# Kernel optimization log

Measured on AMD Instinct MI355X. Metric: run time of the kernel, lower is better.

Reference implementation:

```python
import jax, jax.numpy as jnp
import numpy as np

B, M, C, D, FF, FEAT = 1, 1024, 128, 512, 1024, 20
PAIR = 3 * D + 2 * FEAT  # slow_scorer_size = 1576


def _ffnn(x, W0, b0, W1, b1):
    # FFNN(depth=1): hidden relu layer then linear output (eval mode, no dropout)
    return jax.nn.relu(x @ W0 + b0) @ W1 + b1


def _batch_gather(x, idx):
    # x: [B, M, ...], idx: [B, ...] int -> gather along mention dim per batch
    return jax.vmap(lambda xb, ib: xb[ib])(x, idx)


def _bucket_distance(d):
    # log-scale distance buckets 0..9 (identity for d<=4)
    log_idx = jnp.floor(jnp.log(jnp.maximum(d, 1).astype(jnp.float32)) / jnp.log(2.0)).astype(jnp.int32) + 3
    return jnp.clip(jnp.where(d <= 4, d, log_idx), 0, 9)


def setup_inputs() -> dict:
    key = jax.random.key(0)
    ks = jax.random.split(key, 10)
    s = 0.02
    return {
        'mention_emb': jax.random.normal(ks[0], (B, M, D), dtype=jnp.float32),
        'mention_cluster_ids': jax.random.randint(ks[1], (B, M), 0, 200),
        'mention_speaker_ids': jax.random.randint(ks[2], (B, M), 0, 2),
        'ms_W0': jax.random.normal(ks[3], (D, FF), dtype=jnp.float32) * s,
        'ms_b0': jnp.zeros((FF,), jnp.float32),
        'ms_W1': jax.random.normal(ks[4], (FF, 1), dtype=jnp.float32) * s,
        'ms_b1': jnp.zeros((1,), jnp.float32),
        'sp_W0': jax.random.normal(ks[5], (PAIR, FF), dtype=jnp.float32) * s,
        'sp_b0': jnp.zeros((FF,), jnp.float32),
        'sp_W1': jax.random.normal(ks[6], (FF, 1), dtype=jnp.float32) * s,
        'sp_b1': jnp.zeros((1,), jnp.float32),
        'speaker_emb': jax.random.normal(ks[7], (2, FEAT), dtype=jnp.float32) * s,
        'bucket_emb': jax.random.normal(ks[8], (10, FEAT), dtype=jnp.float32) * s,
    }


def reference(mention_emb, mention_cluster_ids, mention_speaker_ids,
              ms_W0, ms_b0, ms_W1, ms_b1,
              sp_W0, sp_b0, sp_W1, sp_b1,
              speaker_emb, bucket_emb):
    # mention scoring
    mention_scores = _ffnn(mention_emb, ms_W0, ms_b0, ms_W1, ms_b1)[..., 0]  # [B, M]

    # get_antecedent_info: fixed window of C previous mentions
    offsets = jnp.arange(1, C + 1)[None, None, :]                    # [1,1,C]
    raw = jnp.arange(M)[None, :, None] - offsets                      # [1,M,C]
    antecedents = jnp.broadcast_to(jnp.clip(raw, 0, M - 1), (B, M, C))
    ant_mask = jnp.broadcast_to(raw >= 0, (B, M, C))

    fast_scores = _batch_gather(mention_scores, antecedents) + mention_scores[:, :, None]
    antecedent_emb = _batch_gather(mention_emb, antecedents)          # [B,M,C,D]

    # slow pair scorer features
    same_speaker = (_batch_gather(mention_speaker_ids, antecedents) == mention_speaker_ids[:, :, None]).astype(jnp.int32)
    speaker_feat = speaker_emb[same_speaker]                          # [B,M,C,FEAT]
    bucket_feat = jnp.broadcast_to(bucket_emb[_bucket_distance(offsets)], (B, M, C, FEAT))

    src = jnp.broadcast_to(mention_emb[:, :, None, :], (B, M, C, D))
    pair_emb = jnp.concatenate([src, antecedent_emb, src * antecedent_emb, speaker_feat, bucket_feat], axis=-1)
    slow_scores = _ffnn(pair_emb, sp_W0, sp_b0, sp_W1, sp_b1)[..., 0]  # [B,M,C]

    antecedent_scores = fast_scores + slow_scores + jnp.log(ant_mask.astype(jnp.float32))
    overall_scores = jnp.concatenate([jnp.zeros((B, M, 1), jnp.float32), antecedent_scores], axis=2)
    overall_dist = jax.nn.softmax(overall_scores, axis=-1)
    eps = 1e-6
    overall_dist = jnp.clip(overall_dist, eps, 1.0 - eps)
    overall_dist = overall_dist / jnp.sum(overall_dist, axis=-1, keepdims=True)

    # coref loss from cluster ids
    ant_cluster = _batch_gather(mention_cluster_ids, antecedents) * ant_mask.astype(mention_cluster_ids.dtype)
    same_cluster = ant_cluster == mention_cluster_ids[:, :, None]
    non_dummy = (mention_cluster_ids > 0)[:, :, None]
    ant_labels = same_cluster & non_dummy
    dummy_labels = ~jnp.any(ant_labels, axis=2, keepdims=True)
    overall_labels = jnp.concatenate([dummy_labels, ant_labels], axis=2)
    loss = -jnp.sum(jnp.log(overall_dist) * overall_labels.astype(jnp.float32), axis=2)
    loss = jnp.mean(jnp.sum(loss, axis=1))
    return overall_dist, loss
```

## Files before the change

kernel.cpp:

```cpp
#include <hip/hip_runtime.h>
#include <math.h>

#define MM 1024
#define DD 512
#define CC 128
#define LDSR 516


typedef __attribute__((ext_vector_type(8))) short bf16x8;
typedef __attribute__((ext_vector_type(4), aligned(8))) short bf16x4a;
typedef __attribute__((ext_vector_type(4))) float f32x4;
typedef __attribute__((ext_vector_type(16))) float f32x16;

__device__ __forceinline__ ushort bf16_rn(float x) {
    uint u = __float_as_uint(x);
    uint r = u + 0x7fffu + ((u >> 16) & 1u);
    return (ushort)(r >> 16);
}
__device__ __forceinline__ float bf16_to_f(ushort u) {
    return __uint_as_float(((uint)u) << 16);
}
__device__ __forceinline__ bf16x8 ld_lds16(const ushort* p) {
    bf16x4a lo = *(const bf16x4a*)p;
    bf16x4a hi = *(const bf16x4a*)(p + 4);
    return __builtin_shufflevector(lo, hi, 0, 1, 2, 3, 4, 5, 6, 7);
}

__global__ __launch_bounds__(256) void prep_emb(const float* __restrict__ emb,
                                                ushort* __restrict__ embb)
{
    int i = blockIdx.x * 256 + threadIdx.x;
    float2 v = ((const float2*)emb)[i];
    ushort2 o;
    o.x = bf16_rn(v.x);
    o.y = bf16_rn(v.y);
    ((ushort2*)embb)[i] = o;
}

__global__ __launch_bounds__(256) void prep_wall(const float* __restrict__ ms_W0,
                                                 const float* __restrict__ sp_W0,
                                                 ushort* __restrict__ Wall)
{
    __shared__ float t[64][65];
    const int k0 = blockIdx.x * 64;
    const int n0 = blockIdx.y * 64;
    const int g = n0 >> 10;
    const float* src = (g == 0) ? ms_W0 : (sp_W0 + (size_t)(g - 1) * 512 * 1024);
    const int col0 = n0 & 1023;
    const int tr = threadIdx.x >> 6, tc = threadIdx.x & 63;
#pragma unroll
    for (int i = 0; i < 16; ++i) {
        int k = tr + i * 4;
        t[k][tc] = src[(size_t)(k0 + k) * 1024 + col0 + tc];
    }
    __syncthreads();
    const int f = threadIdx.x >> 2;
    const int c4 = threadIdx.x & 3;
    ushort tmp[16];
#pragma unroll
    for (int j = 0; j < 16; ++j) tmp[j] = bf16_rn(t[c4 * 16 + j][f]);
    uint4* dst = (uint4*)(Wall + (size_t)(n0 + f) * 512 + k0 + c4 * 16);
    dst[0] = *(uint4*)&tmp[0];
    dst[1] = *(uint4*)&tmp[8];
}

__global__ __launch_bounds__(64) void prep_wfrag(const float* __restrict__ W,
                                                 ushort* __restrict__ dst_frag)
{
    const int ts = blockIdx.x;
    const int l = threadIdx.x;
    const int tt = ts >> 5, s = ts & 31;
    const int f = tt * 32 + (l & 31);
    const int kb = s * 16 + (l >> 5) * 8;
    ushort tmp[8];
#pragma unroll
    for (int j = 0; j < 8; ++j) tmp[j] = bf16_rn(W[(size_t)(kb + j) * 1024 + f]);
    uint4* dst = (uint4*)(dst_frag + ((size_t)ts * 64 + l) * 8);
    *dst = *(uint4*)&tmp[0];
}

__global__ __launch_bounds__(256) void gemm_h_mfma(
    const ushort* __restrict__ embb, const ushort* __restrict__ Wall,
    float* __restrict__ H)
{
    const int n0 = blockIdx.x * 128;
    const int m0 = blockIdx.y * 128;
    const int lane = threadIdx.x & 63, wave = threadIdx.x >> 6;
    const int wx = wave & 1, wy = wave >> 1;
    const int l15 = lane & 15, lq = lane >> 4;

    const ushort* arow[4];
#pragma unroll
    for (int mi = 0; mi < 4; ++mi)
        arow[mi] = embb + (size_t)(m0 + wy * 64 + mi * 16 + l15) * 512;
    const ushort* brow[4];
#pragma unroll
    for (int ni = 0; ni < 4; ++ni)
        brow[ni] = Wall + (size_t)(n0 + wx * 64 + ni * 16 + l15) * 512;

    f32x4 acc[4][4];
#pragma unroll
    for (int i = 0; i < 4; ++i)
#pragma unroll
        for (int j = 0; j < 4; ++j) acc[i][j] = (f32x4)0.f;

    for (int kt = 0; kt < 512; kt += 32) {
        const int ko = kt + lq * 8;
        bf16x8 av[4], bv[4];
#pragma unroll
        for (int mi = 0; mi < 4; ++mi) av[mi] = *(const bf16x8*)(arow[mi] + ko);
#pragma unroll
        for (int ni = 0; ni < 4; ++ni) bv[ni] = *(const bf16x8*)(brow[ni] + ko);
#pragma unroll
        for (int mi = 0; mi < 4; ++mi)
#pragma unroll
            for (int ni = 0; ni < 4; ++ni)
                acc[mi][ni] = __builtin_amdgcn_mfma_f32_16x16x32_bf16(av[mi], bv[ni], acc[mi][ni], 0, 0, 0);
    }
#pragma unroll
    for (int mi = 0; mi < 4; ++mi)
#pragma unroll
        for (int r = 0; r < 4; ++r) {
            int mrow = m0 + wy * 64 + mi * 16 + lq * 4 + r;
#pragma unroll
            for (int ni = 0; ni < 4; ++ni)
                H[(size_t)mrow * 3072 + n0 + wx * 64 + ni * 16 + l15] = acc[mi][ni][r];
        }
}

__global__ void small_proj(const float* __restrict__ speaker_emb,
                           const float* __restrict__ bucket_emb,
                           const float* __restrict__ sp_W0,
                           float* __restrict__ spk_proj, float* __restrict__ bkt_proj)
{
    int r = blockIdx.x;
    const float* e; const float* W; float* out;
    if (r < 2) { e = speaker_emb + r * 20; W = sp_W0 + (size_t)1536 * 1024; out = spk_proj + r * 1024; }
    else       { e = bucket_emb + (r - 2) * 20; W = sp_W0 + (size_t)1556 * 1024; out = bkt_proj + (r - 2) * 1024; }
    float ek[20];
#pragma unroll
    for (int k = 0; k < 20; ++k) ek[k] = e[k];
    for (int f = threadIdx.x; f < 1024; f += blockDim.x) {
        float s = 0.f;
#pragma unroll
        for (int k = 0; k < 20; ++k) s = fmaf(ek[k], W[(size_t)k * 1024 + f], s);
        out[f] = s;
    }
}

__global__ __launch_bounds__(256) void mention_score(
    const float* __restrict__ H, const float* __restrict__ ms_b0,
    const float* __restrict__ ms_W1, const float* __restrict__ ms_b1,
    float* __restrict__ ms)
{
    int m = blockIdx.x;
    float v = 0.f;
    for (int f = threadIdx.x; f < 1024; f += 256) {
        float h = H[(size_t)m * 3072 + f] + ms_b0[f];
        v += fmaxf(h, 0.f) * ms_W1[f];
    }
#pragma unroll
    for (int o = 1; o < 64; o <<= 1) v += __shfl_xor(v, o);
    __shared__ float sm[4];
    if ((threadIdx.x & 63) == 0) sm[threadIdx.x >> 6] = v;
    __syncthreads();
    if (threadIdx.x == 0) ms[m] = sm[0] + sm[1] + sm[2] + sm[3] + ms_b1[0];
}

__global__ __launch_bounds__(512, 4) void pair_mfma(
    const ushort* __restrict__ embb, const ushort* __restrict__ Wfrag,
    const float* __restrict__ H, const float* __restrict__ spk_proj,
    const float* __restrict__ bkt_proj, const float* __restrict__ sp_b0,
    const float* __restrict__ sp_W1, const int* __restrict__ speaker,
    float* __restrict__ slow0, float* __restrict__ slow1)
{
    extern __shared__ ushort Alds[];
    float* red = (float*)(Alds + 64 * LDSR);
    int* meta_ss = (int*)(red + 8 * 64);
    int* meta_bk = meta_ss + 64;
    const int m = blockIdx.x;
    const int cbase = (blockIdx.y & 1) * 64;
    const int fh = blockIdx.y >> 1;
    const int tid = threadIdx.x;
    const int spk_m = speaker[m];

    {
        const int c = tid & 63;
        const int kh = (tid >> 6) * 64;
        int a = m - 1 - (cbase + c); if (a < 0) a = 0;
        const ushort* ea = embb + (size_t)a * 512 + kh;
        const ushort* em = embb + (size_t)m * 512 + kh;
        ushort* dst = Alds + c * LDSR + kh;
#pragma unroll
        for (int j = 0; j < 64; j += 8) {
            bf16x8 va = *(const bf16x8*)(ea + j);
            bf16x8 vm = *(const bf16x8*)(em + j);
            uint pr[4];
#pragma unroll
            for (int p = 0; p < 4; ++p) {
                float q0 = bf16_to_f((ushort)va[2 * p])     * bf16_to_f((ushort)vm[2 * p]);
                float q1 = bf16_to_f((ushort)va[2 * p + 1]) * bf16_to_f((ushort)vm[2 * p + 1]);
                pr[p] = __builtin_amdgcn_perm(__float_as_uint(q1), __float_as_uint(q0), 0x07060302u);
            }
            *(uint2*)(dst + j)     = *(uint2*)&pr[0];
            *(uint2*)(dst + j + 4) = *(uint2*)&pr[2];
        }
        if (tid < 64) {
            meta_ss[c] = (speaker[a] == spk_m) ? 1 : 0;
            int off = cbase + c + 1;
            int bk;
            if (off <= 4) bk = off;
            else { bk = 31 - __clz(off) + 3; if (bk > 9) bk = 9; }
            meta_bk[c] = bk;
        }
    }
    __syncthreads();

    const int lane = tid & 63;
    const int wave = __builtin_amdgcn_readfirstlane(tid >> 6);
    const int l31 = lane & 31, k5 = lane >> 5;

    const int f0 = fh * 512 + wave * 64;
    const ushort* bb = Wfrag + (size_t)(fh * 16 + wave * 2) * 16384 + (size_t)lane * 8;
    const ushort* ab = Alds + l31 * LDSR + k5 * 8;

    f32x16 acc[2][2];
#pragma unroll
    for (int i = 0; i < 2; ++i)
#pragma unroll
        for (int j = 0; j < 2; ++j) acc[i][j] = (f32x16)0.f;

#pragma unroll 2
    for (int s = 0; s < 32; ++s) {
        bf16x8 b0 = *(const bf16x8*)(bb + s * 512);
        bf16x8 b1 = *(const bf16x8*)(bb + 16384 + s * 512);
        bf16x8 a0 = ld_lds16(ab + s * 16);
        bf16x8 a1 = ld_lds16(ab + 32 * LDSR + s * 16);
        __builtin_amdgcn_s_setprio(1);
        acc[0][0] = __builtin_amdgcn_mfma_f32_32x32x16_bf16(a0, b0, acc[0][0], 0, 0, 0);
        acc[0][1] = __builtin_amdgcn_mfma_f32_32x32x16_bf16(a0, b1, acc[0][1], 0, 0, 0);
        acc[1][0] = __builtin_amdgcn_mfma_f32_32x32x16_bf16(a1, b0, acc[1][0], 0, 0, 0);
        acc[1][1] = __builtin_amdgcn_mfma_f32_32x32x16_bf16(a1, b1, acc[1][1], 0, 0, 0);
        __builtin_amdgcn_s_setprio(0);
    }

    float srcb[2], w1v[2], sp0v[2], sp1v[2];
#pragma unroll
    for (int ni = 0; ni < 2; ++ni) {
        int fcol = f0 + ni * 32 + l31;
        srcb[ni] = H[(size_t)m * 3072 + 1024 + fcol] + sp_b0[fcol];
        w1v[ni]  = sp_W1[fcol];
        sp0v[ni] = spk_proj[fcol];
        sp1v[ni] = spk_proj[1024 + fcol];
    }
#pragma unroll
    for (int mi = 0; mi < 2; ++mi) {
#pragma unroll
        for (int reg = 0; reg < 16; ++reg) {
            const int c = mi * 32 + 4 * k5 + (reg & 3) + 8 * (reg >> 2);
            int a = m - 1 - (cbase + c); if (a < 0) a = 0;
            const int ss = meta_ss[c];
            const int bk = meta_bk[c];
            const float* antp = H + (size_t)a * 3072 + 2048;
            float s = 0.f;
#pragma unroll
            for (int ni = 0; ni < 2; ++ni) {
                const int fcol = f0 + ni * 32 + l31;
                float bval = bkt_proj[(size_t)bk * 1024 + fcol];
                float pre = acc[mi][ni][reg] + srcb[ni] + antp[fcol] + (ss ? sp1v[ni] : sp0v[ni]) + bval;
                s += fmaxf(pre, 0.f) * w1v[ni];
            }
            s += __shfl_xor(s, 1); s += __shfl_xor(s, 2); s += __shfl_xor(s, 4);
            s += __shfl_xor(s, 8); s += __shfl_xor(s, 16);
            if (l31 == 0) red[wave * 64 + c] = s;
        }
    }
    __syncthreads();
    if (tid < 64) {
        float s = 0.f;
#pragma unroll
        for (int i = 0; i < 8; ++i) s += red[i * 64 + tid];
        float* sout = fh ? slow1 : slow0;
        sout[(size_t)m * 128 + cbase + tid] = s;
    }
}

__device__ __forceinline__ float bsum2(float v, float* sm) {
#pragma unroll
    for (int o = 1; o < 64; o <<= 1) v += __shfl_xor(v, o);
    __syncthreads();
    if ((threadIdx.x & 63) == 0) sm[threadIdx.x >> 6] = v;
    __syncthreads();
    return sm[0] + sm[1];
}
__device__ __forceinline__ float bmax2(float v, float* sm) {
#pragma unroll
    for (int o = 1; o < 64; o <<= 1) v = fmaxf(v, __shfl_xor(v, o));
    __syncthreads();
    if ((threadIdx.x & 63) == 0) sm[threadIdx.x >> 6] = v;
    __syncthreads();
    return fmaxf(sm[0], sm[1]);
}

__global__ __launch_bounds__(128) void softmax_loss(
    const float* __restrict__ slow0, const float* __restrict__ slow1,
    const float* __restrict__ ms,
    const float* __restrict__ sp_b1, const int* __restrict__ cluster,
    float* __restrict__ out, float* __restrict__ loss_partial)
{
    const int m = blockIdx.x, c = threadIdx.x;
    __shared__ float sm[2];
    const int raw = m - 1 - c;
    const bool maskv = raw >= 0;
    const int a = maskv ? raw : 0;
    float score = slow0[(size_t)m * 128 + c] + slow1[(size_t)m * 128 + c]
                + sp_b1[0] + ms[m] + ms[a];
    if (!maskv) score = -INFINITY;

    float mx = fmaxf(bmax2(score, sm), 0.f);
    float e = expf(score - mx);
    float e0 = expf(0.f - mx);
    float sum = bsum2(e, sm) + e0;
    float p = e / sum, p0 = e0 / sum;
    const float eps = 1e-6f;
    p  = fminf(fmaxf(p,  eps), 1.f - eps);
    p0 = fminf(fmaxf(p0, eps), 1.f - eps);
    float sum2 = bsum2(p, sm) + p0;
    p /= sum2; p0 /= sum2;
    out[(size_t)m * 129 + 1 + c] = p;
    if (c == 0) out[(size_t)m * 129] = p0;

    const int cid = cluster[m];
    const bool lbl = maskv && (cid > 0) && (cluster[a] == cid);
    float anyc = bsum2(lbl ? 1.f : 0.f, sm);
    float lsum = bsum2(lbl ? -logf(p) : 0.f, sm);
    if (c == 0) {
        if (anyc == 0.f) lsum += -logf(p0);
        loss_partial[m] = lsum;
    }
}

__global__ void loss_sum(const float* __restrict__ lp, float* __restrict__ out) {
    float v = 0.f;
    for (int i = threadIdx.x; i < 1024; i += 256) v += lp[i];
#pragma unroll
    for (int o = 1; o < 64; o <<= 1) v += __shfl_xor(v, o);
    __shared__ float sm[4];
    if ((threadIdx.x & 63) == 0) sm[threadIdx.x >> 6] = v;
    __syncthreads();
    if (threadIdx.x == 0) out[(size_t)1024 * 129] = sm[0] + sm[1] + sm[2] + sm[3];
}

extern "C" void kernel_launch(void* const* d_in, const int* in_sizes, int n_in,
                              void* d_out, int out_size, void* d_ws, size_t ws_size,
                              hipStream_t stream)
{
    const float* emb   = (const float*)d_in[0];
    const int*   clus  = (const int*)  d_in[1];
    const int*   spk   = (const int*)  d_in[2];
    const float* ms_W0 = (const float*)d_in[3];
    const float* ms_b0 = (const float*)d_in[4];
    const float* ms_W1 = (const float*)d_in[5];
    const float* ms_b1 = (const float*)d_in[6];
    const float* sp_W0 = (const float*)d_in[7];
    const float* sp_b0 = (const float*)d_in[8];
    const float* sp_W1 = (const float*)d_in[9];
    const float* sp_b1 = (const float*)d_in[10];
    const float* spke  = (const float*)d_in[11];
    const float* bkte  = (const float*)d_in[12];

    float* ws = (float*)d_ws;
    float* H        = ws;
    float* slow0    = ws + 3145728;
    float* spk_proj = ws + 3276800;
    float* bkt_proj = ws + 3278848;
    float* msc      = ws + 3289088;
    float* lossp    = ws + 3290112;
    ushort* embb    = (ushort*)(ws + 3291136);
    ushort* Wall    = (ushort*)(ws + 3553280);
    ushort* Wfrag   = Wall + (size_t)3072 * 512;
    float* slow1    = ws + 4601856;
    float* out = (float*)d_out;

    const int pair_lds = 64 * LDSR * 2 + 8 * 64 * 4 + 2 * 64 * 4;

    static bool attr_set = false;
    if (!attr_set) {
        hipFuncSetAttribute((const void*)&pair_mfma,
                            hipFuncAttributeMaxDynamicSharedMemorySize,
                            pair_lds);
        attr_set = true;
    }

    hipLaunchKernelGGL(prep_emb, dim3(1024), dim3(256), 0, stream, emb, embb);
    hipLaunchKernelGGL(prep_wall, dim3(8, 48), dim3(256), 0, stream, ms_W0, sp_W0, Wall);
    hipLaunchKernelGGL(prep_wfrag, dim3(1024), dim3(64), 0, stream,
                       sp_W0 + (size_t)1024 * 1024, Wfrag);
    hipLaunchKernelGGL(gemm_h_mfma, dim3(24, 8), dim3(256), 0, stream, embb, Wall, H);
    hipLaunchKernelGGL(small_proj, dim3(12), dim3(256), 0, stream, spke, bkte, sp_W0, spk_proj, bkt_proj);
    hipLaunchKernelGGL(mention_score, dim3(1024), dim3(256), 0, stream, H, ms_b0, ms_W1, ms_b1, msc);
    hipLaunchKernelGGL(pair_mfma, dim3(1024, 4), dim3(512), pair_lds, stream,
                       embb, Wfrag, H, spk_proj, bkt_proj, sp_b0, sp_W1, spk, slow0, slow1);
    hipLaunchKernelGGL(softmax_loss, dim3(1024), dim3(128), 0, stream,
                       slow0, slow1, msc, sp_b1, clus, out, lossp);
    hipLaunchKernelGGL(loss_sum, dim3(1), dim3(256), 0, stream, lossp, out);
}
```

Before: 367.3 us.

## Merge two antecedent halves into one 1024-thread pair block; widen LDS rows for 16B loads

The pair kernel now has each block handle all 128 antecedents for one mention and feature half, using 16 waves instead of 8, so each wave's W fragment is shared by two wave groups within the block. This halves the grid and the per-block launch/setup overhead. The LDS row pitch changes from 516 to 520 so A-operand reads and writes can be single 16-byte accesses instead of split 8-byte ones. Doubling the block size and LDS footprint (about 140KB) reduces how many blocks fit per CU and may change bank-conflict behavior.

After: 403.0 us. +9.7%, slower.

```diff
diff --git a/kernel.cpp b/kernel.cpp
--- a/kernel.cpp
+++ b/kernel.cpp
@@ -4,11 +4,10 @@
 #define MM 1024
 #define DD 512
 #define CC 128
-#define LDSR 516
+#define LDSR 520
 
 
 typedef __attribute__((ext_vector_type(8))) short bf16x8;
-typedef __attribute__((ext_vector_type(4), aligned(8))) short bf16x4a;
 typedef __attribute__((ext_vector_type(4))) float f32x4;
 typedef __attribute__((ext_vector_type(16))) float f32x16;
 
@@ -21,9 +20,7 @@
     return __uint_as_float(((uint)u) << 16);
 }
 __device__ __forceinline__ bf16x8 ld_lds16(const ushort* p) {
-    bf16x4a lo = *(const bf16x4a*)p;
-    bf16x4a hi = *(const bf16x4a*)(p + 4);
-    return __builtin_shufflevector(lo, hi, 0, 1, 2, 3, 4, 5, 6, 7);
+    return *(const bf16x8*)__builtin_assume_aligned(p, 16);
 }
 
 __global__ __launch_bounds__(256) void prep_emb(const float* __restrict__ emb,
@@ -167,7 +164,7 @@
     if (threadIdx.x == 0) ms[m] = sm[0] + sm[1] + sm[2] + sm[3] + ms_b1[0];
 }
 
-__global__ __launch_bounds__(512, 4) void pair_mfma(
+__global__ __launch_bounds__(1024, 4) void pair_mfma(
     const ushort* __restrict__ embb, const ushort* __restrict__ Wfrag,
     const float* __restrict__ H, const float* __restrict__ spk_proj,
     const float* __restrict__ bkt_proj, const float* __restrict__ sp_b0,
@@ -175,19 +172,18 @@
     float* __restrict__ slow0, float* __restrict__ slow1)
 {
     extern __shared__ ushort Alds[];
-    float* red = (float*)(Alds + 64 * LDSR);
-    int* meta_ss = (int*)(red + 8 * 64);
-    int* meta_bk = meta_ss + 64;
+    float* red = (float*)(Alds + 128 * LDSR);
+    int* meta_ss = (int*)(red + 16 * 64);
+    int* meta_bk = meta_ss + 128;
     const int m = blockIdx.x;
-    const int cbase = (blockIdx.y & 1) * 64;
-    const int fh = blockIdx.y >> 1;
+    const int fh = blockIdx.y;
     const int tid = threadIdx.x;
     const int spk_m = speaker[m];
 
     {
-        const int c = tid & 63;
-        const int kh = (tid >> 6) * 64;
-        int a = m - 1 - (cbase + c); if (a < 0) a = 0;
+        const int c = tid >> 3;
+        const int kh = (tid & 7) * 64;
+        int a = m - 1 - c; if (a < 0) a = 0;
         const ushort* ea = embb + (size_t)a * 512 + kh;
         const ushort* em = embb + (size_t)m * 512 + kh;
         ushort* dst = Alds + c * LDSR + kh;
@@ -202,12 +198,11 @@
                 float q1 = bf16_to_f((ushort)va[2 * p + 1]) * bf16_to_f((ushort)vm[2 * p + 1]);
                 pr[p] = __builtin_amdgcn_perm(__float_as_uint(q1), __float_as_uint(q0), 0x07060302u);
             }
-            *(uint2*)(dst + j)     = *(uint2*)&pr[0];
-            *(uint2*)(dst + j + 4) = *(uint2*)&pr[2];
+            *(uint4*)__builtin_assume_aligned(dst + j, 16) = *(uint4*)&pr[0];
         }
-        if (tid < 64) {
+        if ((tid & 7) == 0) {
             meta_ss[c] = (speaker[a] == spk_m) ? 1 : 0;
-            int off = cbase + c + 1;
+            int off = c + 1;
             int bk;
             if (off <= 4) bk = off;
             else { bk = 31 - __clz(off) + 3; if (bk > 9) bk = 9; }
@@ -218,11 +213,12 @@
 
     const int lane = tid & 63;
     const int wave = __builtin_amdgcn_readfirstlane(tid >> 6);
+    const int wc = wave >> 3, wf = wave & 7;
     const int l31 = lane & 31, k5 = lane >> 5;
 
-    const int f0 = fh * 512 + wave * 64;
-    const ushort* bb = Wfrag + (size_t)(fh * 16 + wave * 2) * 16384 + (size_t)lane * 8;
-    const ushort* ab = Alds + l31 * LDSR + k5 * 8;
+    const int f0 = fh * 512 + wf * 64;
+    const ushort* bb = Wfrag + (size_t)(fh * 16 + wf * 2) * 16384 + (size_t)lane * 8;
+    const ushort* ab = Alds + (wc * 64 + l31) * LDSR + k5 * 8;
 
     f32x16 acc[2][2];
 #pragma unroll
@@ -257,8 +253,9 @@
     for (int mi = 0; mi < 2; ++mi) {
 #pragma unroll
         for (int reg = 0; reg < 16; ++reg) {
-            const int c = mi * 32 + 4 * k5 + (reg & 3) + 8 * (reg >> 2);
-            int a = m - 1 - (cbase + c); if (a < 0) a = 0;
+            const int cl = mi * 32 + 4 * k5 + (reg & 3) + 8 * (reg >> 2);
+            const int c = wc * 64 + cl;
+            int a = m - 1 - c; if (a < 0) a = 0;
             const int ss = meta_ss[c];
             const int bk = meta_bk[c];
             const float* antp = H + (size_t)a * 3072 + 2048;
@@ -272,16 +269,18 @@
             }
             s += __shfl_xor(s, 1); s += __shfl_xor(s, 2); s += __shfl_xor(s, 4);
             s += __shfl_xor(s, 8); s += __shfl_xor(s, 16);
-            if (l31 == 0) red[wave * 64 + c] = s;
+            if (l31 == 0) red[wave * 64 + cl] = s;
         }
     }
     __syncthreads();
-    if (tid < 64) {
+    if (tid < 128) {
+        const int c = tid;
+        const int wcc = c >> 6, cl = c & 63;
         float s = 0.f;
 #pragma unroll
-        for (int i = 0; i < 8; ++i) s += red[i * 64 + tid];
+        for (int i = 0; i < 8; ++i) s += red[(wcc * 8 + i) * 64 + cl];
         float* sout = fh ? slow1 : slow0;
-        sout[(size_t)m * 128 + cbase + tid] = s;
+        sout[(size_t)m * 128 + c] = s;
     }
 }
 
@@ -382,7 +381,7 @@
     float* slow1    = ws + 4601856;
     float* out = (float*)d_out;
 
-    const int pair_lds = 64 * LDSR * 2 + 8 * 64 * 4 + 2 * 64 * 4;
+    const int pair_lds = 128 * LDSR * 2 + 16 * 64 * 4 + 2 * 128 * 4;
 
     static bool attr_set = false;
     if (!attr_set) {
@@ -399,7 +398,7 @@
     hipLaunchKernelGGL(gemm_h_mfma, dim3(24, 8), dim3(256), 0, stream, embb, Wall, H);
     hipLaunchKernelGGL(small_proj, dim3(12), dim3(256), 0, stream, spke, bkte, sp_W0, spk_proj, bkt_proj);
     hipLaunchKernelGGL(mention_score, dim3(1024), dim3(256), 0, stream, H, ms_b0, ms_W1, ms_b1, msc);
-    hipLaunchKernelGGL(pair_mfma, dim3(1024, 4), dim3(512), pair_lds, stream,
+    hipLaunchKernelGGL(pair_mfma, dim3(1024, 2), dim3(1024), pair_lds, stream,
                        embb, Wfrag, H, spk_proj, bkt_proj, sp_b0, sp_W1, spk, slow0, slow1);
     hipLaunchKernelGGL(softmax_loss, dim3(1024), dim3(128), 0, stream,
                        slow0, slow1, msc, sp_b1, clus, out, lossp);
```

## Retile pair kernel to 32-antecedent blocks using 16x16x32 MFMA

Applied to the files above, without the earlier changes.

The pair-scoring kernel now handles 32 antecedents per block instead of 64, doubling the grid, and switches from 32x32x16 to 16x16x32 bf16 MFMA. Weight fragments are repacked to match, and each wave loops over two 32-feature sub-tiles, accumulating into the shared reduction buffer. The goal is smaller LDS and register footprint for higher occupancy (launch bounds raised to 8 blocks) and a cheaper epilogue. The cost is that each weight fragment is now reloaded by twice as many blocks, which adds global/L2 traffic.

Result: no change. 360.8 us (-1.8%).

```diff
diff --git a/kernel.cpp b/kernel.cpp
--- a/kernel.cpp
+++ b/kernel.cpp
@@ -10,7 +10,6 @@
 typedef __attribute__((ext_vector_type(8))) short bf16x8;
 typedef __attribute__((ext_vector_type(4), aligned(8))) short bf16x4a;
 typedef __attribute__((ext_vector_type(4))) float f32x4;
-typedef __attribute__((ext_vector_type(16))) float f32x16;
 
 __device__ __forceinline__ ushort bf16_rn(float x) {
     uint u = __float_as_uint(x);
@@ -64,14 +63,14 @@
     dst[1] = *(uint4*)&tmp[8];
 }
 
-__global__ __launch_bounds__(64) void prep_wfrag(const float* __restrict__ W,
-                                                 ushort* __restrict__ dst_frag)
+__global__ __launch_bounds__(64) void prep_wfrag16(const float* __restrict__ W,
+                                                   ushort* __restrict__ dst_frag)
 {
     const int ts = blockIdx.x;
     const int l = threadIdx.x;
-    const int tt = ts >> 5, s = ts & 31;
-    const int f = tt * 32 + (l & 31);
-    const int kb = s * 16 + (l >> 5) * 8;
+    const int t16 = ts >> 4, s = ts & 15;
+    const int f = t16 * 16 + (l & 15);
+    const int kb = s * 32 + ((l >> 4) & 3) * 8;
     ushort tmp[8];
 #pragma unroll
     for (int j = 0; j < 8; ++j) tmp[j] = bf16_rn(W[(size_t)(kb + j) * 1024 + f]);
@@ -167,32 +166,33 @@
     if (threadIdx.x == 0) ms[m] = sm[0] + sm[1] + sm[2] + sm[3] + ms_b1[0];
 }
 
-__global__ __launch_bounds__(512, 4) void pair_mfma(
-    const ushort* __restrict__ embb, const ushort* __restrict__ Wfrag,
+__global__ __launch_bounds__(512, 8) void pair_mfma(
+    const ushort* __restrict__ embb, const ushort* __restrict__ Wfrag16,
     const float* __restrict__ H, const float* __restrict__ spk_proj,
     const float* __restrict__ bkt_proj, const float* __restrict__ sp_b0,
     const float* __restrict__ sp_W1, const int* __restrict__ speaker,
     float* __restrict__ slow0, float* __restrict__ slow1)
 {
     extern __shared__ ushort Alds[];
-    float* red = (float*)(Alds + 64 * LDSR);
-    int* meta_ss = (int*)(red + 8 * 64);
-    int* meta_bk = meta_ss + 64;
+    float* red = (float*)(Alds + 32 * LDSR);
+    int* meta_ss = (int*)(red + 8 * 32);
+    int* meta_bk = meta_ss + 32;
     const int m = blockIdx.x;
-    const int cbase = (blockIdx.y & 1) * 64;
-    const int fh = blockIdx.y >> 1;
+    const int cq = blockIdx.y & 3;
+    const int fh = blockIdx.y >> 2;
+    const int cbase = cq * 32;
     const int tid = threadIdx.x;
     const int spk_m = speaker[m];
 
     {
-        const int c = tid & 63;
-        const int kh = (tid >> 6) * 64;
+        const int c = tid & 31;
+        const int kh = (tid >> 5) * 32;
         int a = m - 1 - (cbase + c); if (a < 0) a = 0;
         const ushort* ea = embb + (size_t)a * 512 + kh;
         const ushort* em = embb + (size_t)m * 512 + kh;
         ushort* dst = Alds + c * LDSR + kh;
 #pragma unroll
-        for (int j = 0; j < 64; j += 8) {
+        for (int j = 0; j < 32; j += 8) {
             bf16x8 va = *(const bf16x8*)(ea + j);
             bf16x8 vm = *(const bf16x8*)(em + j);
             uint pr[4];
@@ -205,7 +205,7 @@
             *(uint2*)(dst + j)     = *(uint2*)&pr[0];
             *(uint2*)(dst + j + 4) = *(uint2*)&pr[2];
         }
-        if (tid < 64) {
+        if (tid < 32) {
             meta_ss[c] = (speaker[a] == spk_m) ? 1 : 0;
             int off = cbase + c + 1;
             int bk;
@@ -218,68 +218,75 @@
 
     const int lane = tid & 63;
     const int wave = __builtin_amdgcn_readfirstlane(tid >> 6);
-    const int l31 = lane & 31, k5 = lane >> 5;
-
-    const int f0 = fh * 512 + wave * 64;
-    const ushort* bb = Wfrag + (size_t)(fh * 16 + wave * 2) * 16384 + (size_t)lane * 8;
-    const ushort* ab = Alds + l31 * LDSR + k5 * 8;
-
-    f32x16 acc[2][2];
-#pragma unroll
-    for (int i = 0; i < 2; ++i)
-#pragma unroll
-        for (int j = 0; j < 2; ++j) acc[i][j] = (f32x16)0.f;
+    const int l15 = lane & 15, lq = lane >> 4;
+    const ushort* ab0 = Alds + l15 * LDSR + lq * 8;
+
+#pragma unroll 1
+    for (int ft2 = 0; ft2 < 2; ++ft2) {
+        const int f0a = fh * 512 + wave * 64 + ft2 * 32;
+        const ushort* bb0 = Wfrag16 + (size_t)(fh * 32 + wave * 4 + ft2 * 2) * 8192
+                                    + (size_t)lane * 8;
+        f32x4 acc[2][2];
+#pragma unroll
+        for (int i = 0; i < 2; ++i)
+#pragma unroll
+            for (int j = 0; j < 2; ++j) acc[i][j] = (f32x4)0.f;
 
 #pragma unroll 2
-    for (int s = 0; s < 32; ++s) {
-        bf16x8 b0 = *(const bf16x8*)(bb + s * 512);
-        bf16x8 b1 = *(const bf16x8*)(bb + 16384 + s * 512);
-        bf16x8 a0 = ld_lds16(ab + s * 16);
-        bf16x8 a1 = ld_lds16(ab + 32 * LDSR + s * 16);
-        __builtin_amdgcn_s_setprio(1);
-        acc[0][0] = __builtin_amdgcn_mfma_f32_32x32x16_bf16(a0, b0, acc[0][0], 0, 0, 0);
-        acc[0][1] = __builtin_amdgcn_mfma_f32_32x32x16_bf16(a0, b1, acc[0][1], 0, 0, 0);
-        acc[1][0] = __builtin_amdgcn_mfma_f32_32x32x16_bf16(a1, b0, acc[1][0], 0, 0, 0);
-        acc[1][1] = __builtin_amdgcn_mfma_f32_32x32x16_bf16(a1, b1, acc[1][1], 0, 0, 0);
-        __builtin_amdgcn_s_setprio(0);
-    }
-
-    float srcb[2], w1v[2], sp0v[2], sp1v[2];
-#pragma unroll
-    for (int ni = 0; ni < 2; ++ni) {
-        int fcol = f0 + ni * 32 + l31;
-        srcb[ni] = H[(size_t)m * 3072 + 1024 + fcol] + sp_b0[fcol];
-        w1v[ni]  = sp_W1[fcol];
-        sp0v[ni] = spk_proj[fcol];
-        sp1v[ni] = spk_proj[1024 + fcol];
-    }
-#pragma unroll
-    for (int mi = 0; mi < 2; ++mi) {
-#pragma unroll
-        for (int reg = 0; reg < 16; ++reg) {
-            const int c = mi * 32 + 4 * k5 + (reg & 3) + 8 * (reg >> 2);
-            int a = m - 1 - (cbase + c); if (a < 0) a = 0;
-            const int ss = meta_ss[c];
-            const int bk = meta_bk[c];
-            const float* antp = H + (size_t)a * 3072 + 2048;
-            float s = 0.f;
-#pragma unroll
-            for (int ni = 0; ni < 2; ++ni) {
-                const int fcol = f0 + ni * 32 + l31;
-                float bval = bkt_proj[(size_t)bk * 1024 + fcol];
-                float pre = acc[mi][ni][reg] + srcb[ni] + antp[fcol] + (ss ? sp1v[ni] : sp0v[ni]) + bval;
-                s += fmaxf(pre, 0.f) * w1v[ni];
+        for (int s = 0; s < 16; ++s) {
+            bf16x8 b0 = *(const bf16x8*)(bb0 + s * 512);
+            bf16x8 b1 = *(const bf16x8*)(bb0 + 8192 + s * 512);
+            bf16x8 a0 = ld_lds16(ab0 + s * 32);
+            bf16x8 a1 = ld_lds16(ab0 + 16 * LDSR + s * 32);
+            __builtin_amdgcn_s_setprio(1);
+            acc[0][0] = __builtin_amdgcn_mfma_f32_16x16x32_bf16(a0, b0, acc[0][0], 0, 0, 0);
+            acc[0][1] = __builtin_amdgcn_mfma_f32_16x16x32_bf16(a0, b1, acc[0][1], 0, 0, 0);
+            acc[1][0] = __builtin_amdgcn_mfma_f32_16x16x32_bf16(a1, b0, acc[1][0], 0, 0, 0);
+            acc[1][1] = __builtin_amdgcn_mfma_f32_16x16x32_bf16(a1, b1, acc[1][1], 0, 0, 0);
+            __builtin_amdgcn_s_setprio(0);
+        }
+
+        float srcb[2], w1v[2], sp0v[2], sp1v[2];
+#pragma unroll
+        for (int fi = 0; fi < 2; ++fi) {
+            int fcol = f0a + fi * 16 + l15;
+            srcb[fi] = H[(size_t)m * 3072 + 1024 + fcol] + sp_b0[fcol];
+            w1v[fi]  = sp_W1[fcol];
+            sp0v[fi] = spk_proj[fcol];
+            sp1v[fi] = spk_proj[1024 + fcol];
+        }
+#pragma unroll
+        for (int ct = 0; ct < 2; ++ct) {
+#pragma unroll
+            for (int reg = 0; reg < 4; ++reg) {
+                const int cl = ct * 16 + lq * 4 + reg;
+                int a = m - 1 - (cbase + cl); if (a < 0) a = 0;
+                const int ss = meta_ss[cl];
+                const int bk = meta_bk[cl];
+                const float* antp = H + (size_t)a * 3072 + 2048;
+                float s = 0.f;
+#pragma unroll
+                for (int fi = 0; fi < 2; ++fi) {
+                    const int fcol = f0a + fi * 16 + l15;
+                    float bval = bkt_proj[(size_t)bk * 1024 + fcol];
+                    float pre = acc[ct][fi][reg] + srcb[fi] + antp[fcol]
+                              + (ss ? sp1v[fi] : sp0v[fi]) + bval;
+                    s += fmaxf(pre, 0.f) * w1v[fi];
+                }
+                s += __shfl_xor(s, 1); s += __shfl_xor(s, 2);
+                s += __shfl_xor(s, 4); s += __shfl_xor(s, 8);
+                if (l15 == 0) {
+                    if (ft2 == 0) red[wave * 32 + cl] = s;
+                    else          red[wave * 32 + cl] += s;
+                }
             }
-            s += __shfl_xor(s, 1); s += __shfl_xor(s, 2); s += __shfl_xor(s, 4);
-            s += __shfl_xor(s, 8); s += __shfl_xor(s, 16);
-            if (l31 == 0) red[wave * 64 + c] = s;
-        }
-    }
-    __syncthreads();
-    if (tid < 64) {
+        }
+    }
+    __syncthreads();
+    if (tid < 32) {
         float s = 0.f;
 #pragma unroll
-        for (int i = 0; i < 8; ++i) s += red[i * 64 + tid];
+        for (int i = 0; i < 8; ++i) s += red[i * 32 + tid];
         float* sout = fh ? slow1 : slow0;
         sout[(size_t)m * 128 + cbase + tid] = s;
     }
@@ -378,11 +385,11 @@
     float* lossp    = ws + 3290112;
     ushort* embb    = (ushort*)(ws + 3291136);
     ushort* Wall    = (ushort*)(ws + 3553280);
-    ushort* Wfrag   = Wall + (size_t)3072 * 512;
+    ushort* Wfrag16 = Wall + (size_t)3072 * 512;
     float* slow1    = ws + 4601856;
     float* out = (float*)d_out;
 
-    const int pair_lds = 64 * LDSR * 2 + 8 * 64 * 4 + 2 * 64 * 4;
+    const int pair_lds = 32 * LDSR * 2 + 8 * 32 * 4 + 2 * 32 * 4;
 
     static bool attr_set = false;
     if (!attr_set) {
@@ -394,13 +401,13 @@
 
     hipLaunchKernelGGL(prep_emb, dim3(1024), dim3(256), 0, stream, emb, embb);
     hipLaunchKernelGGL(prep_wall, dim3(8, 48), dim3(256), 0, stream, ms_W0, sp_W0, Wall);
-    hipLaunchKernelGGL(prep_wfrag, dim3(1024), dim3(64), 0, stream,
-                       sp_W0 + (size_t)1024 * 1024, Wfrag);
+    hipLaunchKernelGGL(prep_wfrag16, dim3(1024), dim3(64), 0, stream,
+                       sp_W0 + (size_t)1024 * 1024, Wfrag16);
     hipLaunchKernelGGL(gemm_h_mfma, dim3(24, 8), dim3(256), 0, stream, embb, Wall, H);
     hipLaunchKernelGGL(small_proj, dim3(12), dim3(256), 0, stream, spke, bkte, sp_W0, spk_proj, bkt_proj);
     hipLaunchKernelGGL(mention_score, dim3(1024), dim3(256), 0, stream, H, ms_b0, ms_W1, ms_b1, msc);
-    hipLaunchKernelGGL(pair_mfma, dim3(1024, 4), dim3(512), pair_lds, stream,
-                       embb, Wfrag, H, spk_proj, bkt_proj, sp_b0, sp_W1, spk, slow0, slow1);
+    hipLaunchKernelGGL(pair_mfma, dim3(1024, 8), dim3(512), pair_lds, stream,
+                       embb, Wfrag16, H, spk_proj, bkt_proj, sp_b0, sp_W1, spk, slow0, slow1);
     hipLaunchKernelGGL(softmax_loss, dim3(1024), dim3(128), 0, stream,
                        slow0, slow1, msc, sp_b1, clus, out, lossp);
     hipLaunchKernelGGL(loss_sum, dim3(1), dim3(256), 0, stream, lossp, out);
```
